# Kernel optimization log

Measured on AMD Instinct MI355X. Metric: run time of the kernel, lower is better.

The kernel has to match this reference:

```python
import jax, jax.numpy as jnp
import numpy as np

STATE_DIM = 13
HIDDEN = 1024
NUM_SENSORS = 32
BATCH = 131072


def _sensor_locations():
    # Replicates the torch buffer construction (linspace over theta/phi on a sphere of radius 2)
    sensor_range = 2.0
    theta = np.linspace(0.0, 2.0 * np.pi, NUM_SENSORS // 2, dtype=np.float64)
    phi = np.linspace(0.0, np.pi, 2, dtype=np.float64)
    sensors = []
    for p in phi:
        for t in theta:
            sensors.append([sensor_range * np.sin(p) * np.cos(t),
                            sensor_range * np.sin(p) * np.sin(t),
                            sensor_range * np.cos(p)])
    return jnp.asarray(np.asarray(sensors[:NUM_SENSORS], dtype=np.float32))


def setup_inputs() -> dict:
    key = jax.random.key(0)
    ks = jax.random.split(key, 24)

    def lin(kw, fan_in, fan_out):
        # torch nn.Linear default init: U(-1/sqrt(fan_in), 1/sqrt(fan_in))
        bound = 1.0 / np.sqrt(fan_in)
        w = jax.random.uniform(kw, (fan_in, fan_out), jnp.float32, -bound, bound)
        return w

    def bias(kb, fan_in, fan_out):
        bound = 1.0 / np.sqrt(fan_in)
        return jax.random.uniform(kb, (fan_out,), jnp.float32, -bound, bound)

    branch_in = NUM_SENSORS * (STATE_DIM + 4)  # 544
    h2, h4, h8 = HIDDEN // 2, HIDDEN // 4, HIDDEN // 8
    inp = {
        "state": jax.random.normal(ks[0], (BATCH, STATE_DIM), jnp.float32),
        "action": jax.random.normal(ks[1], (BATCH, 4), jnp.float32),
        "sensor_locations": _sensor_locations(),
        "bw1": lin(ks[2], branch_in, HIDDEN), "bb1": bias(ks[3], branch_in, HIDDEN),
        "bw2": lin(ks[4], HIDDEN, h2), "bb2": bias(ks[5], HIDDEN, h2),
        "bw3": lin(ks[6], h2, h4), "bb3": bias(ks[7], h2, h4),
        "tw1": lin(ks[8], 3, h4), "tb1": bias(ks[9], 3, h4),
        "tw2": lin(ks[10], h4, h4), "tb2": bias(ks[11], h4, h4),
        "qw1": lin(ks[12], 3, h8), "qb1": bias(ks[13], 3, h8),
        "qw2": lin(ks[14], h8, STATE_DIM), "qb2": bias(ks[15], h8, STATE_DIM),
        "pw": lin(ks[16], h4, STATE_DIM), "pb": bias(ks[17], h4, STATE_DIM),
        "residual_weight": jnp.float32(0.1),
    }
    return inp


def reference(state, action, sensor_locations,
              bw1, bb1, bw2, bb2, bw3, bb3,
              tw1, tb1, tw2, tb2,
              qw1, qb1, qw2, qb2,
              pw, pb, residual_weight):
    B = state.shape[0]
    pos = state[:, :3]

    # Vectorized sensor encoding (replaces the 32-iteration python loop):
    # distance [B, S, 1], weight = exp(-d/0.5)
    diff = sensor_locations[None, :, :] - pos[:, None, :]          # [B, S, 3]
    dist = jnp.linalg.norm(diff, axis=-1, keepdims=True)           # [B, S, 1]
    w = jnp.exp(-dist / 0.5)                                       # [B, S, 1]
    sv = jnp.concatenate([state[:, None, :] * w,
                          action[:, None, :] * w], axis=-1)        # [B, S, sd+4]
    enc = sv.reshape(B, -1)                                        # [B, S*(sd+4)]

    # Branch net (dropout is identity in eval mode)
    h = jax.nn.relu(enc @ bw1 + bb1)
    h = jax.nn.relu(h @ bw2 + bb2)
    branch = h @ bw3 + bb3                                         # [B, hidden//4]

    # Trunk net on eval coords
    t = jnp.tanh(pos @ tw1 + tb1)
    trunk = jnp.tanh(t @ tw2 + tb2)                                # [B, hidden//4]

    interaction = branch * trunk
    output_delta = interaction @ pw + pb                           # [B, state_dim]

    b = jax.nn.relu(pos @ qw1 + qb1)
    bias_out = b @ qw2 + qb2                                       # [B, state_dim]

    next_state = state + residual_weight * (output_delta + bias_out)

    # Quaternion normalization for dims 3:7 (state_dim >= 7)
    quat = next_state[:, 3:7]
    qn = jnp.linalg.norm(quat, axis=1, keepdims=True)
    next_state = next_state.at[:, 3:7].set(quat / (qn + 1e-8))
    return next_state
```

## Files before the change

### kernel.cpp

```cpp
#include <hip/hip_runtime.h>
#include <hip/hip_bf16.h>
#include <hip/hip_fp8.h>

#define B_TOTAL 131072

typedef __attribute__((ext_vector_type(8))) short short8;
typedef __attribute__((ext_vector_type(4))) float f32x4;
typedef __attribute__((ext_vector_type(16))) unsigned char uchar16;
typedef __attribute__((ext_vector_type(4))) int int4v;
typedef __attribute__((ext_vector_type(8))) int int8v;
typedef unsigned int uint;

#define MFMA(a,b,c) __builtin_amdgcn_mfma_f32_16x16x32_bf16(a,b,c,0,0,0)
#define MFMA8(a,b,c) __builtin_amdgcn_mfma_f32_16x16x32_fp8_fp8(a,b,c,0,0,0)
#define MFMAS(a,b,c) __builtin_amdgcn_mfma_scale_f32_16x16x128_f8f6f4( \
    a, b, c, 0, 0, 0, 0x7F7F7F7F, 0, 0x7F7F7F7F)

union V8U { int8v v; int4v h[2]; };

__device__ __forceinline__ short f2bf(float f) {
  union { float f; uint u; } x; x.f = f;
  uint r = x.u + 0x7fffu + ((x.u >> 16) & 1u);
  return (short)(r >> 16);
}
__device__ __forceinline__ unsigned char f2fp8(float v) {
  union { __hip_fp8_e4m3 q; unsigned char b; } u;
  u.q = __hip_fp8_e4m3(v);
  return u.b;
}
__device__ __forceinline__ float ftanh(float x) {
  float e = __builtin_amdgcn_exp2f(x * 2.8853900817779268f);
  return 1.f - 2.f * __builtin_amdgcn_rcpf(e + 1.f);
}

__device__ __forceinline__ void gl_lds16(const void* g, void* l) {
  __builtin_amdgcn_global_load_lds((const __attribute__((address_space(1))) uint*)g,
                                   (__attribute__((address_space(3))) uint*)l, 16, 0, 0);
}
__device__ __forceinline__ int swz8(int c, int r) { return (c & ~7) | ((c ^ r) & 7); }

__global__ __launch_bounds__(256)
void prep(const float* __restrict__ bw1, const float* __restrict__ bw2,
          const float* __restrict__ bw3, const float* __restrict__ tw2,
          const float* __restrict__ pw, const float* __restrict__ qw2,
          unsigned char* __restrict__ w1r, unsigned char* __restrict__ w2r,
          unsigned char* __restrict__ w3r, short* __restrict__ w4r,
          short* __restrict__ pwT, short* __restrict__ qw2T) {
  __shared__ float tile[32][33];
  int b = blockIdx.x;
  if (b == 1344) {
    for (int t = threadIdx.x; t < 6144; t += 256) {
      if (t < 4096) { int c = t >> 8, k = t & 255;
        pwT[t] = (c < 13) ? f2bf(pw[k * 13 + c]) : (short)0; }
      else { int i = t - 4096; int c = i >> 7, j = i & 127;
        qw2T[i] = (c < 13) ? f2bf(qw2[j * 13 + c]) : (short)0; }
    }
    return;
  }
  const float* src; int K, N, mat;
  if (b < 640)       { src = bw1; K = 544;  N = 1024; mat = 0; }
  else if (b < 1152) { b -= 640;  src = bw2; K = 1024; N = 512;  mat = 1; }
  else if (b < 1280) { b -= 1152; src = bw3; K = 512;  N = 256;  mat = 2; }
  else               { b -= 1280; src = tw2; K = 256;  N = 256;  mat = 3; }
  const int ntk = (mat == 0) ? 20 : (mat == 1) ? 32 : (mat == 2) ? 16 : 8;
  const int tn = b / ntk, tk = b % ntk;
  const int k0 = tk * 32, n0 = tn * 32;
  const int tx = threadIdx.x & 31, ty = threadIdx.x >> 5;
#pragma unroll
  for (int rr = 0; rr < 32; rr += 8) {
    int k = k0 + ty + rr;
    tile[ty + rr][tx] = (k < K) ? src[(long)k * N + n0 + tx] : 0.f;
  }
  __syncthreads();
#pragma unroll
  for (int rr = 0; rr < 32; rr += 8) {
    int nl = ty + rr;
    int n = n0 + nl, k = k0 + tx;
    float v = tile[tx][nl];
    if (mat == 0 || mat == 1) {
      const int NTk = (mat == 0) ? 5 : 8;
      unsigned char* dst = (mat == 0) ? w1r : w2r;
      const long rec = (long)(n >> 4) * NTk + (k >> 7);
      const int ln = ((k >> 5) & 3) * 16 + (n & 15);
      dst[rec * 2048 + ln * 32 + (k & 31)] = f2fp8(v);
    } else {
      int ks = k >> 5, fq = (k >> 3) & 3, j = k & 7;
      int wb = n >> 5, hf = (n >> 4) & 1, fr = n & 15;
      long idx = (long)(((ks * 8 + wb) * 2 + hf) * 4 + fq) * 128 + fr * 8 + j;
      if (mat == 2) w3r[idx] = f2fp8(v);
      else          w4r[idx] = f2bf(v);
    }
  }
}

__global__ __launch_bounds__(256)
void enc_k(const float* __restrict__ state, const float* __restrict__ action,
           const float* __restrict__ sensors, unsigned char* __restrict__ enc) {
  __shared__ float sval[64][17];
  __shared__ float wexp[64][32];
  __shared__ float sens[96];
  const int tid = threadIdx.x;
  const int rb = blockIdx.x * 64;
  if (tid < 96) sens[tid] = sensors[tid];
  for (int i = tid; i < 64 * 17; i += 256) {
    const int r = i / 17, c = i % 17;
    const long grow = rb + r;
    sval[r][c] = (c < 13) ? state[grow * 13 + c] : action[grow * 4 + (c - 13)];
  }
  __syncthreads();
  for (int i = tid; i < 64 * 32; i += 256) {
    const int r = i >> 5, s = i & 31;
    const float dx = sens[s*3+0] - sval[r][0];
    const float dy = sens[s*3+1] - sval[r][1];
    const float dz = sens[s*3+2] - sval[r][2];
    wexp[r][s] = __expf(-2.0f * sqrtf(dx*dx + dy*dy + dz*dz));
  }
  __syncthreads();
  for (int i = tid; i < 64 * 40; i += 256) {
    const int r = i / 40, c16 = i % 40;
    uchar16 v;
#pragma unroll
    for (int j = 0; j < 16; ++j) {
      const int k = c16 * 16 + j;
      unsigned char o = 0;
      if (k < 544) { const int s = k / 17, c = k % 17; o = f2fp8(sval[r][c] * wexp[r][s]); }
      v[j] = o;
    }
    *(uchar16*)&enc[((long)(rb + r)) * 640 + c16 * 16] = v;
  }
}

template<int N, int K, int ACT>
__global__ __launch_bounds__(256, 2)
void gemm_mx(const unsigned char* __restrict__ A, const unsigned char* __restrict__ Br,
             const float* __restrict__ bias, unsigned char* __restrict__ C) {
  constexpr int NT = K / 128;
  constexpr int NTN = N / 128;
  __shared__ __align__(16) unsigned char As[2][128 * 128];
  const int tid = threadIdx.x;
  const int wave = tid >> 6;
  const int lane = tid & 63;
  const int Mtiles = gridDim.x / NTN;
  const int bid = blockIdx.x;
  const int xcd = bid & 7, seq = bid >> 3;
  const int tm = xcd * (Mtiles >> 3) + seq / NTN;
  const int tn = seq % NTN;
  const long arow0 = (long)tm * 128;
  const long brow0 = (long)tn * 128;

  const int wr = (wave >> 1) * 64;
  const int wc = (wave & 1) * 64;
  const int fr = lane & 15;
  const int fg = lane >> 4;

  auto stageA = [&](int b, int kt) {
    const int k0 = kt * 128;
#pragma unroll
    for (int it = 0; it < 4; ++it) {
      const int ch = it * 256 + tid;
      const int row = ch >> 3;
      const int cs = (ch & 7) ^ (row & 7);
      gl_lds16(A + (arow0 + row) * (long)K + k0 + cs * 16, &As[b][ch * 16]);
    }
  };

  const unsigned char* bbase = Br + ((long)(tn * 8 + (wc >> 4)) * NT) * 2048 + lane * 32;
  int8v bvb[2][4];
  auto bload = [&](int buf, int kt) {
#pragma unroll
    for (int n = 0; n < 4; ++n) {
      const unsigned char* p = bbase + ((long)n * NT + kt) * 2048;
      V8U u;
      u.h[0] = *(const int4v*)p;
      u.h[1] = *(const int4v*)(p + 16);
      bvb[buf][n] = u.v;
    }
  };

  f32x4 acc[4][4] = {};

  stageA(0, 0);
  bload(0, 0);
#pragma unroll
  for (int kt = 0; kt < NT; ++kt) {
    const int cur = kt & 1;
    __syncthreads();
    if (kt + 1 < NT) { stageA(cur ^ 1, kt + 1); bload(cur ^ 1, kt + 1); }
    const unsigned char* Ab = As[cur];
    int8v av[4];
#pragma unroll
    for (int m = 0; m < 4; ++m) {
      const int row = wr + m * 16 + fr;
      const int p0 = (2 * fg) ^ (row & 7);
      V8U u;
      u.h[0] = *(const int4v*)&Ab[row * 128 + (p0 << 4)];
      u.h[1] = *(const int4v*)&Ab[row * 128 + ((p0 ^ 1) << 4)];
      av[m] = u.v;
    }
#pragma unroll
    for (int m = 0; m < 4; ++m)
#pragma unroll
      for (int n = 0; n < 4; ++n)
        acc[m][n] = MFMAS(av[m], bvb[cur][n], acc[m][n]);
  }

  float bv[4];
#pragma unroll
  for (int n = 0; n < 4; ++n) bv[n] = bias[tn * 128 + wc + n * 16 + fr];
#pragma unroll
  for (int m = 0; m < 4; ++m)
#pragma unroll
    for (int n = 0; n < 4; ++n) {
      const long col = brow0 + wc + n * 16 + fr;
#pragma unroll
      for (int r = 0; r < 4; ++r) {
        const long row = arow0 + wr + m * 16 + fg * 4 + r;
        float v = acc[m][n][r] + bv[n];
        if (ACT == 1) v = fmaxf(v, 0.f);
        C[row * (long)N + col] = f2fp8(v);
      }
    }
}

__global__ __launch_bounds__(512, 4)
void k2(const unsigned char* __restrict__ h2, const float* __restrict__ state,
        const float* __restrict__ tw1, const float* __restrict__ tb1,
        const unsigned char* __restrict__ w3r, const float* __restrict__ bb3,
        const short* __restrict__ w4r, const float* __restrict__ tb2,
        const short* __restrict__ pwT, const float* __restrict__ qw1,
        const short* __restrict__ qw2T, const float* __restrict__ qb1,
        const float* __restrict__ pb, const float* __restrict__ qb2,
        const float* __restrict__ rwp, float* __restrict__ out) {
  __shared__ __align__(16) char lds[77824];
  char*  h2S = lds;
  short* tS  = (short*)(lds + 32768);
  short* pwS = (short*)(lds + 65536);
  short* q2S = (short*)(lds + 73728);
  float* prS = (float*)(lds + 16384);
  float* pr2S= (float*)(lds + 20480);

  const int tid = threadIdx.x, wave = tid >> 6, lane = tid & 63;
  const int fr = lane & 15, fg = lane >> 4;
  const long rb = (long)blockIdx.x * 64;

#pragma unroll
  for (int it = 0; it < 4; ++it) {
    int ch = it * 512 + tid;
    int row = ch >> 5, c = ch & 31;
    gl_lds16(h2 + (rb + row) * 512 + ((c ^ (row & 7)) << 4), h2S + ch * 16);
  }
  { int row = tid >> 5, c = tid & 31;
    gl_lds16(pwT + (long)row * 256 + swz8(c, row) * 8, (char*)pwS + tid * 16); }
  if (tid < 256) { int row = tid >> 4, c = tid & 15;
    gl_lds16(qw2T + (long)row * 128 + swz8(c, row) * 8, (char*)q2S + tid * 16); }

  long long bb[4][2];
#pragma unroll
  for (int ks = 0; ks < 4; ++ks) {
    bb[ks][0] = *(const long long*)&w3r[(long)((ks * 8 + wave) * 2 + 0) * 512 + lane * 8];
    bb[ks][1] = *(const long long*)&w3r[(long)((ks * 8 + wave) * 2 + 1) * 512 + lane * 8];
  }

  for (int i = tid; i < 64 * 32; i += 512) {
    int r = i >> 5, c8 = i & 31;
    float p0 = state[(rb + r) * 13 + 0], p1 = state[(rb + r) * 13 + 1], p2 = state[(rb + r) * 13 + 2];
    short8 v;
#pragma unroll
    for (int j = 0; j < 8; ++j) {
      int jj = c8 * 8 + j;
      v[j] = f2bf(ftanh(p0 * tw1[jj] + p1 * tw1[256 + jj] + p2 * tw1[512 + jj] + tb1[jj]));
    }
    *(short8*)&tS[(r * 32 + swz8(c8, r)) * 8] = v;
  }
  __syncthreads();

  f32x4 acc3[4][2] = {};
#pragma unroll
  for (int ks = 0; ks < 16; ++ks) {
    long long a[4];
#pragma unroll
    for (int mf = 0; mf < 4; ++mf) {
      int row = mf * 16 + fr;
      int c16 = (ks * 2 + (fg >> 1)) ^ (row & 7);
      a[mf] = *(const long long*)&h2S[row * 512 + (c16 << 4) + ((fg & 1) << 3)];
    }
    const long long c0 = bb[ks & 3][0], c1 = bb[ks & 3][1];
    if (ks + 4 < 16) {
      bb[ks & 3][0] = *(const long long*)&w3r[(long)(((ks + 4) * 8 + wave) * 2 + 0) * 512 + lane * 8];
      bb[ks & 3][1] = *(const long long*)&w3r[(long)(((ks + 4) * 8 + wave) * 2 + 1) * 512 + lane * 8];
    }
#pragma unroll
    for (int mf = 0; mf < 4; ++mf) {
      acc3[mf][0] = MFMA8(a[mf], c0, acc3[mf][0]);
      acc3[mf][1] = MFMA8(a[mf], c1, acc3[mf][1]);
    }
  }

  short8 bb4[2][2];
#pragma unroll
  for (int ks = 0; ks < 2; ++ks) {
    bb4[ks][0] = *(const short8*)&w4r[(long)((ks * 8 + wave) * 2 + 0) * 512 + lane * 8];
    bb4[ks][1] = *(const short8*)&w4r[(long)((ks * 8 + wave) * 2 + 1) * 512 + lane * 8];
  }
  f32x4 accT[4][2] = {};
#pragma unroll
  for (int ks = 0; ks < 8; ++ks) {
    const short8 c0 = bb4[ks & 1][0], c1 = bb4[ks & 1][1];
    if (ks + 2 < 8) {
      bb4[ks & 1][0] = *(const short8*)&w4r[(long)(((ks + 2) * 8 + wave) * 2 + 0) * 512 + lane * 8];
      bb4[ks & 1][1] = *(const short8*)&w4r[(long)(((ks + 2) * 8 + wave) * 2 + 1) * 512 + lane * 8];
    }
#pragma unroll
    for (int mf = 0; mf < 4; ++mf) {
      int row = mf * 16 + fr;
      short8 aF = *(const short8*)&tS[row * 256 + swz8(ks * 4 + fg, row) * 8];
      accT[mf][0] = MFMA(aF, c0, accT[mf][0]);
      accT[mf][1] = MFMA(aF, c1, accT[mf][1]);
    }
  }
  __syncthreads();

#pragma unroll
  for (int nf = 0; nf < 2; ++nf) {
    int col = wave * 32 + nf * 16 + fr;
    float b3 = bb3[col], t2 = tb2[col];
#pragma unroll
    for (int mf = 0; mf < 4; ++mf)
#pragma unroll
      for (int i = 0; i < 4; ++i) {
        int row = mf * 16 + fg * 4 + i;
        float br = acc3[mf][nf][i] + b3;
        float tr = ftanh(accT[mf][nf][i] + t2);
        tS[row * 256 + swz8(col >> 3, row) * 8 + (col & 7)] = f2bf(br * tr);
      }
  }
  __syncthreads();

  if (wave < 4) {
    int row = wave * 16 + fr;
    f32x4 accP = {0.f, 0.f, 0.f, 0.f};
#pragma unroll
    for (int ks = 0; ks < 8; ++ks) {
      short8 a = *(const short8*)&tS[row * 256 + swz8(ks * 4 + fg, row) * 8];
      short8 b = *(const short8*)&pwS[fr * 256 + swz8(ks * 4 + fg, fr) * 8];
      accP = MFMA(a, b, accP);
    }
#pragma unroll
    for (int i = 0; i < 4; ++i)
      prS[(wave * 16 + fg * 4 + i) * 16 + fr] = accP[i];
  } else {
    int row = (wave - 4) * 16 + fr;
    float p0 = state[(rb + row) * 13 + 0], p1 = state[(rb + row) * 13 + 1],
          p2 = state[(rb + row) * 13 + 2];
    f32x4 accQ = {0.f, 0.f, 0.f, 0.f};
#pragma unroll
    for (int ks = 0; ks < 4; ++ks) {
      short8 a;
#pragma unroll
      for (int j = 0; j < 8; ++j) {
        int jj = (ks * 4 + fg) * 8 + j;
        float hv = fmaxf(p0 * qw1[jj] + p1 * qw1[128 + jj] + p2 * qw1[256 + jj] + qb1[jj], 0.f);
        a[j] = f2bf(hv);
      }
      short8 b = *(const short8*)&q2S[fr * 128 + swz8(ks * 4 + fg, fr) * 8];
      accQ = MFMA(a, b, accQ);
    }
#pragma unroll
    for (int i = 0; i < 4; ++i)
      pr2S[((wave - 4) * 16 + fg * 4 + i) * 16 + fr] = accQ[i];
  }
  __syncthreads();

  if (tid < 64) {
    int r = tid;
    float rw = rwp[0];
    float ns[13];
#pragma unroll
    for (int c = 0; c < 13; ++c)
      ns[c] = state[(rb + r) * 13 + c] + rw * (prS[r * 16 + c] + pr2S[r * 16 + c] + pb[c] + qb2[c]);
    float qn = sqrtf(ns[3] * ns[3] + ns[4] * ns[4] + ns[5] * ns[5] + ns[6] * ns[6]) + 1e-8f;
#pragma unroll
    for (int c = 3; c < 7; ++c) ns[c] /= qn;
#pragma unroll
    for (int c = 0; c < 13; ++c) out[(rb + r) * 13 + c] = ns[c];
  }
}

extern "C" void kernel_launch(void* const* d_in, const int* in_sizes, int n_in,
                              void* d_out, int out_size, void* d_ws, size_t ws_size,
                              hipStream_t stream) {
  const float* state  = (const float*)d_in[0];
  const float* action = (const float*)d_in[1];
  const float* sensors= (const float*)d_in[2];
  const float* bw1 = (const float*)d_in[3];
  const float* bb1 = (const float*)d_in[4];
  const float* bw2 = (const float*)d_in[5];
  const float* bb2 = (const float*)d_in[6];
  const float* bw3 = (const float*)d_in[7];
  const float* bb3 = (const float*)d_in[8];
  const float* tw1 = (const float*)d_in[9];
  const float* tb1 = (const float*)d_in[10];
  const float* tw2 = (const float*)d_in[11];
  const float* tb2 = (const float*)d_in[12];
  const float* qw1 = (const float*)d_in[13];
  const float* qb1 = (const float*)d_in[14];
  const float* qw2 = (const float*)d_in[15];
  const float* qb2 = (const float*)d_in[16];
  const float* pw  = (const float*)d_in[17];
  const float* pb  = (const float*)d_in[18];
  const float* rw  = (const float*)d_in[19];
  float* out = (float*)d_out;

  char* p = (char*)d_ws;
  unsigned char* w1r = (unsigned char*)p; p += (size_t)1024 * 640;
  unsigned char* w2r = (unsigned char*)p; p += (size_t)512 * 1024;
  unsigned char* w3r = (unsigned char*)p; p += (size_t)256 * 512;
  short* w4r = (short*)p;          p += (size_t)256 * 256 * 2;
  short* pwT = (short*)p;          p += (size_t)16 * 256 * 2;
  short* qw2T= (short*)p;          p += (size_t)16 * 128 * 2;
  const size_t fixed = (size_t)(p - (char*)d_ws);
  const size_t avail = (ws_size > fixed) ? ws_size - fixed : 0;
  long Mc = (long)(avail / 1664) & ~1023L;
  if (Mc > B_TOTAL) Mc = B_TOTAL;
  if (Mc < 1024) return;
  unsigned char* encb = (unsigned char*)p;
  unsigned char* h2b  = (unsigned char*)p;
  unsigned char* h1f  = (unsigned char*)(p + (size_t)Mc * 640);

  prep<<<dim3(1345), dim3(256), 0, stream>>>(bw1, bw2, bw3, tw2, pw, qw2,
                                             w1r, w2r, w3r, w4r, pwT, qw2T);

  for (long r0 = 0; r0 < B_TOTAL; r0 += Mc) {
    long Mr = B_TOTAL - r0; if (Mr > Mc) Mr = Mc;
    enc_k<<<dim3(Mr / 64), dim3(256), 0, stream>>>(state + r0 * 13, action + r0 * 4,
                                                   sensors, encb);
    gemm_mx<1024, 640, 1><<<dim3((Mr / 128) * 8), dim3(256), 0, stream>>>(
        encb, w1r, bb1, h1f);
    gemm_mx<512, 1024, 1><<<dim3((Mr / 128) * 4), dim3(256), 0, stream>>>(
        h1f, w2r, bb2, h2b);
    k2<<<dim3(Mr / 64), dim3(512), 0, stream>>>(h2b, state + r0 * 13, tw1, tb1,
                                                w3r, bb3, w4r, tb2, pwT, qw1, qw2T,
                                                qb1, pb, qb2, rw, out + r0 * 13);
  }
}
```

Measured before the change: 304.9 us.

## Fuse sensor encoding into first branch GEMM, generating FP8 A tiles in LDS

Removes the separate encoding kernel and the round trip of the 640-byte-per-row FP8 encoding buffer through global memory. The first GEMM now loads state and action for its 128-row tile, computes the sensor weights in LDS, and builds each swizzled FP8 A tile on the fly. Each of the 8 N-tile blocks per row tile recomputes the same encoding, and the larger LDS footprint may lower occupancy. The workspace layout shrinks to h1 plus h2 per row.

New measurement: 618.7 us. 2.03x slower.

```diff
diff --git a/kernel.cpp b/kernel.cpp
--- a/kernel.cpp
+++ b/kernel.cpp
@@ -27,6 +27,13 @@
   union { __hip_fp8_e4m3 q; unsigned char b; } u;
   u.q = __hip_fp8_e4m3(v);
   return u.b;
+}
+__device__ __forceinline__ uint f2fp8x2(float a, float b) {
+#if __has_builtin(__builtin_amdgcn_cvt_pk_fp8_f32)
+  return (uint)__builtin_amdgcn_cvt_pk_fp8_f32(a, b, 0, false) & 0xFFFFu;
+#else
+  return (uint)f2fp8(a) | ((uint)f2fp8(b) << 8);
+#endif
 }
 __device__ __forceinline__ float ftanh(float x) {
   float e = __builtin_amdgcn_exp2f(x * 2.8853900817779268f);
@@ -93,41 +100,128 @@
   }
 }
 
-__global__ __launch_bounds__(256)
-void enc_k(const float* __restrict__ state, const float* __restrict__ action,
-           const float* __restrict__ sensors, unsigned char* __restrict__ enc) {
-  __shared__ float sval[64][17];
-  __shared__ float wexp[64][32];
-  __shared__ float sens[96];
+__global__ __launch_bounds__(256, 2)
+void gemm1e(const float* __restrict__ state, const float* __restrict__ action,
+            const float* __restrict__ sensors, const unsigned char* __restrict__ Br,
+            const float* __restrict__ bias, unsigned char* __restrict__ C) {
+  constexpr int NT = 5;
+  constexpr int NTN = 8;
+  constexpr int N = 1024;
+  __shared__ __align__(16) unsigned char As[2][128 * 128];
+  __shared__ float svalS[128 * 17];
+  __shared__ float wexpS[128 * 32];
+  __shared__ float sensS[96];
   const int tid = threadIdx.x;
-  const int rb = blockIdx.x * 64;
-  if (tid < 96) sens[tid] = sensors[tid];
-  for (int i = tid; i < 64 * 17; i += 256) {
-    const int r = i / 17, c = i % 17;
-    const long grow = rb + r;
-    sval[r][c] = (c < 13) ? state[grow * 13 + c] : action[grow * 4 + (c - 13)];
-  }
-  __syncthreads();
-  for (int i = tid; i < 64 * 32; i += 256) {
-    const int r = i >> 5, s = i & 31;
-    const float dx = sens[s*3+0] - sval[r][0];
-    const float dy = sens[s*3+1] - sval[r][1];
-    const float dz = sens[s*3+2] - sval[r][2];
-    wexp[r][s] = __expf(-2.0f * sqrtf(dx*dx + dy*dy + dz*dz));
-  }
-  __syncthreads();
-  for (int i = tid; i < 64 * 40; i += 256) {
-    const int r = i / 40, c16 = i % 40;
-    uchar16 v;
-#pragma unroll
-    for (int j = 0; j < 16; ++j) {
-      const int k = c16 * 16 + j;
-      unsigned char o = 0;
-      if (k < 544) { const int s = k / 17, c = k % 17; o = f2fp8(sval[r][c] * wexp[r][s]); }
-      v[j] = o;
-    }
-    *(uchar16*)&enc[((long)(rb + r)) * 640 + c16 * 16] = v;
-  }
+  const int wave = tid >> 6;
+  const int lane = tid & 63;
+  const int Mtiles = gridDim.x / NTN;
+  const int bid = blockIdx.x;
+  const int xcd = bid & 7, seq = bid >> 3;
+  const int tm = xcd * (Mtiles >> 3) + seq / NTN;
+  const int tn = seq % NTN;
+  const long arow0 = (long)tm * 128;
+  const long brow0 = (long)tn * 128;
+
+  const int wr = (wave >> 1) * 64;
+  const int wc = (wave & 1) * 64;
+  const int fr = lane & 15;
+  const int fg = lane >> 4;
+
+  if (tid < 96) sensS[tid] = sensors[tid];
+  for (int i = tid; i < 128 * 17; i += 256) {
+    int r = i / 17, c = i % 17;
+    svalS[i] = (c < 13) ? state[(arow0 + r) * 13 + c] : action[(arow0 + r) * 4 + (c - 13)];
+  }
+  __syncthreads();
+  for (int i = tid; i < 128 * 32; i += 256) {
+    int r = i >> 5, s = i & 31;
+    float dx = sensS[s * 3 + 0] - svalS[r * 17 + 0];
+    float dy = sensS[s * 3 + 1] - svalS[r * 17 + 1];
+    float dz = sensS[s * 3 + 2] - svalS[r * 17 + 2];
+    wexpS[i] = __expf(-2.f * sqrtf(dx * dx + dy * dy + dz * dz));
+  }
+
+  auto encstage = [&](int b, int kt) {
+#pragma unroll
+    for (int it = 0; it < 4; ++it) {
+      const int ch = it * 256 + tid;
+      const int row = ch >> 3;
+      const int lc = ch & 7;
+      const int k0 = kt * 128 + lc * 16;
+      int s = k0 / 17, cc = k0 % 17;
+      uint w[4];
+#pragma unroll
+      for (int q = 0; q < 4; ++q) {
+        float f[4];
+#pragma unroll
+        for (int t = 0; t < 4; ++t) {
+          const int k = k0 + q * 4 + t;
+          f[t] = (k < 544) ? svalS[row * 17 + cc] * wexpS[row * 32 + s] : 0.f;
+          if (++cc == 17) { cc = 0; ++s; }
+        }
+        w[q] = f2fp8x2(f[0], f[1]) | (f2fp8x2(f[2], f[3]) << 16);
+      }
+      int4v v = { (int)w[0], (int)w[1], (int)w[2], (int)w[3] };
+      *(int4v*)&As[b][row * 128 + ((lc ^ (row & 7)) << 4)] = v;
+    }
+  };
+
+  const unsigned char* bbase = Br + ((long)(tn * 8 + (wc >> 4)) * NT) * 2048 + lane * 32;
+  int8v bvb[2][4];
+  auto bload = [&](int buf, int kt) {
+#pragma unroll
+    for (int n = 0; n < 4; ++n) {
+      const unsigned char* p = bbase + ((long)n * NT + kt) * 2048;
+      V8U u;
+      u.h[0] = *(const int4v*)p;
+      u.h[1] = *(const int4v*)(p + 16);
+      bvb[buf][n] = u.v;
+    }
+  };
+
+  f32x4 acc[4][4] = {};
+
+  __syncthreads();
+  encstage(0, 0);
+  bload(0, 0);
+#pragma unroll
+  for (int kt = 0; kt < NT; ++kt) {
+    const int cur = kt & 1;
+    __syncthreads();
+    if (kt + 1 < NT) { encstage(cur ^ 1, kt + 1); bload(cur ^ 1, kt + 1); }
+    const unsigned char* Ab = As[cur];
+    int8v av[4];
+#pragma unroll
+    for (int m = 0; m < 4; ++m) {
+      const int row = wr + m * 16 + fr;
+      const int p0 = (2 * fg) ^ (row & 7);
+      V8U u;
+      u.h[0] = *(const int4v*)&Ab[row * 128 + (p0 << 4)];
+      u.h[1] = *(const int4v*)&Ab[row * 128 + ((p0 ^ 1) << 4)];
+      av[m] = u.v;
+    }
+#pragma unroll
+    for (int m = 0; m < 4; ++m)
+#pragma unroll
+      for (int n = 0; n < 4; ++n)
+        acc[m][n] = MFMAS(av[m], bvb[cur][n], acc[m][n]);
+  }
+
+  float bv[4];
+#pragma unroll
+  for (int n = 0; n < 4; ++n) bv[n] = bias[tn * 128 + wc + n * 16 + fr];
+#pragma unroll
+  for (int m = 0; m < 4; ++m)
+#pragma unroll
+    for (int n = 0; n < 4; ++n) {
+      const long col = brow0 + wc + n * 16 + fr;
+#pragma unroll
+      for (int r = 0; r < 4; ++r) {
+        const long row = arow0 + wr + m * 16 + fg * 4 + r;
+        float v = fmaxf(acc[m][n][r] + bv[n], 0.f);
+        C[row * (long)N + col] = f2fp8(v);
+      }
+    }
 }
 
 template<int N, int K, int ACT>
@@ -420,22 +514,19 @@
   short* qw2T= (short*)p;          p += (size_t)16 * 128 * 2;
   const size_t fixed = (size_t)(p - (char*)d_ws);
   const size_t avail = (ws_size > fixed) ? ws_size - fixed : 0;
-  long Mc = (long)(avail / 1664) & ~1023L;
+  long Mc = (long)(avail / 1536) & ~1023L;
   if (Mc > B_TOTAL) Mc = B_TOTAL;
   if (Mc < 1024) return;
-  unsigned char* encb = (unsigned char*)p;
-  unsigned char* h2b  = (unsigned char*)p;
-  unsigned char* h1f  = (unsigned char*)(p + (size_t)Mc * 640);
+  unsigned char* h1f = (unsigned char*)p;
+  unsigned char* h2b = (unsigned char*)(p + (size_t)Mc * 1024);
 
   prep<<<dim3(1345), dim3(256), 0, stream>>>(bw1, bw2, bw3, tw2, pw, qw2,
                                              w1r, w2r, w3r, w4r, pwT, qw2T);
 
   for (long r0 = 0; r0 < B_TOTAL; r0 += Mc) {
     long Mr = B_TOTAL - r0; if (Mr > Mc) Mr = Mc;
-    enc_k<<<dim3(Mr / 64), dim3(256), 0, stream>>>(state + r0 * 13, action + r0 * 4,
-                                                   sensors, encb);
-    gemm_mx<1024, 640, 1><<<dim3((Mr / 128) * 8), dim3(256), 0, stream>>>(
-        encb, w1r, bb1, h1f);
+    gemm1e<<<dim3((Mr / 128) * 8), dim3(256), 0, stream>>>(
+        state + r0 * 13, action + r0 * 4, sensors, w1r, bb1, h1f);
     gemm_mx<512, 1024, 1><<<dim3((Mr / 128) * 4), dim3(256), 0, stream>>>(
         h1f, w2r, bb2, h2b);
     k2<<<dim3(Mr / 64), dim3(512), 0, stream>>>(h2b, state + r0 * 13, tw1, tb1,
```
